# Performance work log

Hardware: AMD Instinct MI355X
Metric: run time of the kernel (lower is better)

## Reference

```python
import jax, jax.numpy as jnp
import numpy as np

N_NODES = 100000
N_ETYPES = 3
N_EDGES = 200000
IN, HID, OUT = 64, 128, 128


def setup_inputs() -> dict:
    key = jax.random.key(0)
    ks = jax.random.split(key, 7)
    x = jax.random.normal(ks[0], (N_NODES, IN), dtype=jnp.float32)
    edge_src = jax.random.randint(ks[1], (N_ETYPES, N_EDGES), 0, N_NODES, dtype=jnp.int32)
    edge_dst = jax.random.randint(ks[2], (N_ETYPES, N_EDGES), 0, N_NODES, dtype=jnp.int32)
    W1 = jax.random.normal(ks[3], (N_ETYPES, IN, HID), dtype=jnp.float32) * 0.05
    b1 = jax.random.normal(ks[4], (N_ETYPES, HID), dtype=jnp.float32) * 0.05
    W2 = jax.random.normal(ks[5], (N_ETYPES, HID, OUT), dtype=jnp.float32) * 0.05
    b2 = jax.random.normal(ks[6], (N_ETYPES, OUT), dtype=jnp.float32) * 0.05
    return {"x": x, "edge_src": edge_src, "edge_dst": edge_dst,
            "W1": W1, "b1": b1, "W2": W2, "b2": b2}


def _hetero_layer(h, edge_src, edge_dst, W, b):
    """Per-etype linear on src feats, mean-reduce per dst per etype, sum across etypes."""
    n = h.shape[0]
    # Wh: [n_etypes, N, H] -- dense per-etype transform (DGL applies Linear to all src nodes)
    Wh = jnp.einsum('nd,edh->enh', h, W) + b[:, None, :]

    def per_etype(Wh_e, src, dst):
        m = Wh_e[src]                                       # gather messages [E, H]
        s = jax.ops.segment_sum(m, dst, num_segments=n)     # scatter-sum   [N, H]
        cnt = jax.ops.segment_sum(jnp.ones((src.shape[0], 1), Wh_e.dtype), dst,
                                  num_segments=n)
        return s / jnp.maximum(cnt, 1.0)                    # mean reduce (0 if no in-edges)

    out = jax.vmap(per_etype)(Wh, edge_src, edge_dst)       # [n_etypes, N, H]
    return out.sum(axis=0)                                  # cross-type 'sum' aggregate


def reference(x, edge_src, edge_dst, W1, b1, W2, b2):
    h = _hetero_layer(x, edge_src, edge_dst, W1, b1)
    h = jax.nn.leaky_relu(h, negative_slope=0.01)
    return _hetero_layer(h, edge_src, edge_dst, W2, b2)
```

## Files before the change

### kernel.cpp

```cpp
#include <hip/hip_runtime.h>

#define NN 100000
#define NETY 3
#define EE 200000
#define DH 128
#define NBINS (NETY * NN)
#define CAP 32
#define SCAT_B ((NETY * EE + 255) / 256)

typedef __attribute__((ext_vector_type(8))) short short8;
typedef __attribute__((ext_vector_type(4))) short short4v;
typedef __attribute__((ext_vector_type(4))) float f32x4;

__device__ __forceinline__ float bf2f(unsigned short u) {
    return __uint_as_float(((unsigned int)u) << 16);
}
__device__ __forceinline__ unsigned short f2bf(float f) {
    unsigned int u = __float_as_uint(f);
    unsigned int r = ((u >> 16) & 1u) + 0x7fffu;
    return (unsigned short)((u + r) >> 16);
}

template <int K3>
__device__ __forceinline__ void wprep_body(const float* __restrict__ W,
                                           unsigned short* __restrict__ Wf, int tid) {
    int l = tid & 63;
    int nfks = tid >> 6;
    int nf = nfks & 7, ks = nfks >> 3;
    int k0 = ks * 32 + (l >> 4) * 8;
    int col = nf * 16 + (l & 15);
    short8 o;
    #pragma unroll
    for (int j = 0; j < 8; ++j)
        o[j] = (short)f2bf(W[(size_t)(k0 + j) * DH + col]);
    *reinterpret_cast<short8*>(Wf + (size_t)tid * 8) = o;
}

__global__ void scatter_wprep_kernel(const int* __restrict__ esrc,
                                     const int* __restrict__ edst,
                                     int* __restrict__ cnt, int* __restrict__ slots,
                                     const float* __restrict__ W1,
                                     const float* __restrict__ W2,
                                     unsigned short* __restrict__ Wf1,
                                     unsigned short* __restrict__ Wf2) {
    const int bid = blockIdx.x;
    if (bid < SCAT_B) {
        int tid = bid * 256 + threadIdx.x;
        if (tid < NETY * EE) {
            int e = tid / EE;
            int bin = e * NN + edst[tid];
            int pos = atomicAdd(&cnt[bin], 1);
            if (pos < CAP) slots[(size_t)bin * CAP + pos] = esrc[tid];
        }
    } else if (bid < SCAT_B + 12) {
        wprep_body<192>(W1, Wf1, (bid - SCAT_B) * 256 + threadIdx.x);
    } else {
        wprep_body<384>(W2, Wf2, (bid - SCAT_B - 12) * 256 + threadIdx.x);
    }
}

template <int DIN, bool BF16IN, bool BF16OUT>
__launch_bounds__(256)
__global__ void fused_layer_kernel(const void* __restrict__ feat_v,
                                   const int* __restrict__ slots,
                                   const int* __restrict__ cnt,
                                   const unsigned short* __restrict__ Wf,
                                   const float* __restrict__ bias,
                                   void* __restrict__ out_v) {
    constexpr int K3 = 3 * DIN;
    constexpr int NK = K3 / 32;
    constexpr int SP = K3 + 8;
    __shared__ unsigned short s_a[32 * SP];
    __shared__ float s_mask[NETY][32];

    const int t = threadIdx.x;
    const int n0 = blockIdx.x * 32;
    const int g = t >> 4, sub = t & 15;

    #pragma unroll
    for (int bi = 0; bi < 6; ++bi) {
        const int b = bi * 16 + g;
        const int nl = b & 31;
        const int e = b >> 5;
        const int bin = e * NN + n0 + nl;
        const int c = cnt[bin];
        const int sb = bin * CAP;
        const float inv = c > 0 ? 1.f / (float)c : 0.f;
        if constexpr (BF16IN) {
            const unsigned short* feat = (const unsigned short*)feat_v;
            float a[8] = {0.f, 0.f, 0.f, 0.f, 0.f, 0.f, 0.f, 0.f};
            for (int i = 0; i < c; ++i) {
                const int s = slots[sb + i];
                short8 u = *reinterpret_cast<const short8*>(feat + (size_t)s * DIN + sub * 8);
                #pragma unroll
                for (int j = 0; j < 8; ++j) {
                    float f = bf2f((unsigned short)u[j]);
                    a[j] += f > 0.f ? f : 0.01f * f;
                }
            }
            short8 o;
            #pragma unroll
            for (int j = 0; j < 8; ++j) o[j] = (short)f2bf(a[j] * inv);
            *reinterpret_cast<short8*>(&s_a[nl * SP + e * DIN + sub * 8]) = o;
        } else {
            const float* feat = (const float*)feat_v;
            float4 a = make_float4(0.f, 0.f, 0.f, 0.f);
            for (int i = 0; i < c; ++i) {
                const int s = slots[sb + i];
                float4 v = *reinterpret_cast<const float4*>(feat + (size_t)s * DIN + sub * 4);
                a.x += v.x; a.y += v.y; a.z += v.z; a.w += v.w;
            }
            short4v o;
            o[0] = (short)f2bf(a.x * inv);
            o[1] = (short)f2bf(a.y * inv);
            o[2] = (short)f2bf(a.z * inv);
            o[3] = (short)f2bf(a.w * inv);
            *reinterpret_cast<short4v*>(&s_a[nl * SP + e * DIN + sub * 4]) = o;
        }
        if (sub == 0) s_mask[e][nl] = c > 0 ? 1.f : 0.f;
    }
    __syncthreads();

    const int wv = t >> 6, l = t & 63;
    const int rowbase = (wv & 1) * 16;
    const int nfbase = (wv >> 1) * 4;
    const int lr = l & 15, lk = l >> 4;

    f32x4 acc[4] = {{0.f,0.f,0.f,0.f},{0.f,0.f,0.f,0.f},{0.f,0.f,0.f,0.f},{0.f,0.f,0.f,0.f}};
    const unsigned short* sa = &s_a[(rowbase + lr) * SP + lk * 8];

    #pragma unroll
    for (int ks = 0; ks < NK; ++ks) {
        short8 af = *reinterpret_cast<const short8*>(sa + ks * 32);
        const unsigned short* wb = Wf + ((size_t)(ks * 8 + nfbase) * 64 + l) * 8;
        #pragma unroll
        for (int nf = 0; nf < 4; ++nf) {
            short8 bf = *reinterpret_cast<const short8*>(wb + (size_t)nf * 64 * 8);
            acc[nf] = __builtin_amdgcn_mfma_f32_16x16x32_bf16(af, bf, acc[nf], 0, 0, 0);
        }
    }

    #pragma unroll
    for (int nf = 0; nf < 4; ++nf) {
        const int col = (nfbase + nf) * 16 + lr;
        const float b0 = bias[0 * DH + col];
        const float b1 = bias[1 * DH + col];
        const float b2 = bias[2 * DH + col];
        #pragma unroll
        for (int v = 0; v < 4; ++v) {
            const int row = rowbase + lk * 4 + v;
            const float val = acc[nf][v] + s_mask[0][row] * b0
                                         + s_mask[1][row] * b1
                                         + s_mask[2][row] * b2;
            if constexpr (BF16OUT)
                ((unsigned short*)out_v)[(size_t)(n0 + row) * DH + col] = f2bf(val);
            else
                ((float*)out_v)[(size_t)(n0 + row) * DH + col] = val;
        }
    }
}

extern "C" void kernel_launch(void* const* d_in, const int* in_sizes, int n_in,
                              void* d_out, int out_size, void* d_ws, size_t ws_size,
                              hipStream_t stream) {
    const float* x   = (const float*)d_in[0];
    const int* esrc  = (const int*)d_in[1];
    const int* edst  = (const int*)d_in[2];
    const float* W1  = (const float*)d_in[3];
    const float* b1  = (const float*)d_in[4];
    const float* W2  = (const float*)d_in[5];
    const float* b2  = (const float*)d_in[6];
    float* out = (float*)d_out;

    int* cnt    = (int*)d_ws;
    int* slots  = cnt + NBINS;
    unsigned short* Wf1 = (unsigned short*)(slots + (size_t)NBINS * CAP);
    unsigned short* Wf2 = Wf1 + 192 * DH;
    unsigned short* h   = Wf2 + 384 * DH;

    hipMemsetAsync(cnt, 0, sizeof(int) * NBINS, stream);

    scatter_wprep_kernel<<<SCAT_B + 12 + 24, 256, 0, stream>>>(
        esrc, edst, cnt, slots, W1, W2, Wf1, Wf2);

    fused_layer_kernel<64, false, true><<<NN / 32, 256, 0, stream>>>(
        x, slots, cnt, Wf1, b1, h);

    fused_layer_kernel<128, true, false><<<NN / 32, 256, 0, stream>>>(
        h, slots, cnt, Wf2, b2, out);
}
```

Before: 248.7 us.

## Convert x to bf16, process one node per thread-group with batched gathers

```diff
diff --git a/kernel.cpp b/kernel.cpp
--- a/kernel.cpp
+++ b/kernel.cpp
@@ -7,6 +7,8 @@
 #define NBINS (NETY * NN)
 #define CAP 32
 #define SCAT_B ((NETY * EE + 255) / 256)
+#define XPREP_T (NN * 64 / 8)
+#define XPREP_B ((XPREP_T + 255) / 256)
 
 typedef __attribute__((ext_vector_type(8))) short short8;
 typedef __attribute__((ext_vector_type(4))) short short4v;
@@ -19,6 +21,9 @@
     unsigned int u = __float_as_uint(f);
     unsigned int r = ((u >> 16) & 1u) + 0x7fffu;
     return (unsigned short)((u + r) >> 16);
+}
+__device__ __forceinline__ float lrelu(float f) {
+    return f > 0.f ? f : 0.01f * f;
 }
 
 template <int K3>
@@ -42,7 +47,9 @@
                                      const float* __restrict__ W1,
                                      const float* __restrict__ W2,
                                      unsigned short* __restrict__ Wf1,
-                                     unsigned short* __restrict__ Wf2) {
+                                     unsigned short* __restrict__ Wf2,
+                                     const float* __restrict__ x,
+                                     unsigned short* __restrict__ xb) {
     const int bid = blockIdx.x;
     if (bid < SCAT_B) {
         int tid = bid * 256 + threadIdx.x;
@@ -54,14 +61,34 @@
         }
     } else if (bid < SCAT_B + 12) {
         wprep_body<192>(W1, Wf1, (bid - SCAT_B) * 256 + threadIdx.x);
+    } else if (bid < SCAT_B + 36) {
+        wprep_body<384>(W2, Wf2, (bid - SCAT_B - 12) * 256 + threadIdx.x);
     } else {
-        wprep_body<384>(W2, Wf2, (bid - SCAT_B - 12) * 256 + threadIdx.x);
-    }
-}
-
-template <int DIN, bool BF16IN, bool BF16OUT>
+        int tid = (bid - SCAT_B - 36) * 256 + threadIdx.x;
+        if (tid < XPREP_T) {
+            const float* p = x + (size_t)tid * 8;
+            float4 v0 = *reinterpret_cast<const float4*>(p);
+            float4 v1 = *reinterpret_cast<const float4*>(p + 4);
+            short8 o;
+            o[0] = (short)f2bf(v0.x); o[1] = (short)f2bf(v0.y);
+            o[2] = (short)f2bf(v0.z); o[3] = (short)f2bf(v0.w);
+            o[4] = (short)f2bf(v1.x); o[5] = (short)f2bf(v1.y);
+            o[6] = (short)f2bf(v1.z); o[7] = (short)f2bf(v1.w);
+            *reinterpret_cast<short8*>(xb + (size_t)tid * 8) = o;
+        }
+    }
+}
+
+__device__ __forceinline__ int get_slot(int slo, const int* __restrict__ slots,
+                                        int sbase, int j) {
+    int v = __shfl(slo, j & 15, 16);
+    if (j >= 16) v = slots[sbase + j];
+    return v;
+}
+
+template <int DIN, bool LRELU_ON, bool BF16OUT>
 __launch_bounds__(256)
-__global__ void fused_layer_kernel(const void* __restrict__ feat_v,
+__global__ void fused_layer_kernel(const unsigned short* __restrict__ feat,
                                    const int* __restrict__ slots,
                                    const int* __restrict__ cnt,
                                    const unsigned short* __restrict__ Wf,
@@ -70,85 +97,156 @@
     constexpr int K3 = 3 * DIN;
     constexpr int NK = K3 / 32;
     constexpr int SP = K3 + 8;
-    __shared__ unsigned short s_a[32 * SP];
-    __shared__ float s_mask[NETY][32];
+    constexpr int CPL = DIN / 16;
+    __shared__ unsigned short s_a[16 * SP];
+    __shared__ float s_mask[NETY][16];
 
     const int t = threadIdx.x;
-    const int n0 = blockIdx.x * 32;
+    const int n0 = blockIdx.x * 16;
     const int g = t >> 4, sub = t & 15;
-
-    #pragma unroll
-    for (int bi = 0; bi < 6; ++bi) {
-        const int b = bi * 16 + g;
-        const int nl = b & 31;
-        const int e = b >> 5;
-        const int bin = e * NN + n0 + nl;
-        const int c = cnt[bin];
-        const int sb = bin * CAP;
-        const float inv = c > 0 ? 1.f / (float)c : 0.f;
-        if constexpr (BF16IN) {
-            const unsigned short* feat = (const unsigned short*)feat_v;
-            float a[8] = {0.f, 0.f, 0.f, 0.f, 0.f, 0.f, 0.f, 0.f};
-            for (int i = 0; i < c; ++i) {
-                const int s = slots[sb + i];
-                short8 u = *reinterpret_cast<const short8*>(feat + (size_t)s * DIN + sub * 8);
+    const int node = n0 + g;
+
+    int cb[NETY], sl[NETY];
+    #pragma unroll
+    for (int e = 0; e < NETY; ++e) cb[e] = cnt[e * NN + node];
+    #pragma unroll
+    for (int e = 0; e < NETY; ++e)
+        sl[e] = slots[(size_t)(e * NN + node) * CAP + sub];
+
+    int sidx[NETY][4];
+    float wgt[NETY][4];
+    #pragma unroll
+    for (int e = 0; e < NETY; ++e) {
+        const int c = cb[e];
+        const int cm1 = c > 0 ? c - 1 : 0;
+        #pragma unroll
+        for (int j = 0; j < 4; ++j) {
+            const int jj = j < c ? j : cm1;
+            int sv = __shfl(sl[e], jj, 16);
+            sidx[e][j] = c > 0 ? sv : 0;
+            wgt[e][j] = j < c ? 1.f : 0.f;
+        }
+    }
+
+    float a[NETY][CPL];
+    #pragma unroll
+    for (int e = 0; e < NETY; ++e)
+        #pragma unroll
+        for (int k = 0; k < CPL; ++k) a[e][k] = 0.f;
+
+    if constexpr (CPL == 8) {
+        short8 u[NETY][4];
+        #pragma unroll
+        for (int e = 0; e < NETY; ++e)
+            #pragma unroll
+            for (int j = 0; j < 4; ++j)
+                u[e][j] = *reinterpret_cast<const short8*>(
+                    feat + (size_t)sidx[e][j] * DIN + sub * 8);
+        #pragma unroll
+        for (int e = 0; e < NETY; ++e)
+            #pragma unroll
+            for (int j = 0; j < 4; ++j)
                 #pragma unroll
-                for (int j = 0; j < 8; ++j) {
-                    float f = bf2f((unsigned short)u[j]);
-                    a[j] += f > 0.f ? f : 0.01f * f;
+                for (int k = 0; k < 8; ++k) {
+                    float f = bf2f((unsigned short)u[e][j][k]);
+                    if constexpr (LRELU_ON) f = lrelu(f);
+                    a[e][k] = fmaf(wgt[e][j], f, a[e][k]);
+                }
+    } else {
+        short4v u[NETY][4];
+        #pragma unroll
+        for (int e = 0; e < NETY; ++e)
+            #pragma unroll
+            for (int j = 0; j < 4; ++j)
+                u[e][j] = *reinterpret_cast<const short4v*>(
+                    feat + (size_t)sidx[e][j] * DIN + sub * 4);
+        #pragma unroll
+        for (int e = 0; e < NETY; ++e)
+            #pragma unroll
+            for (int j = 0; j < 4; ++j)
+                #pragma unroll
+                for (int k = 0; k < 4; ++k) {
+                    float f = bf2f((unsigned short)u[e][j][k]);
+                    if constexpr (LRELU_ON) f = lrelu(f);
+                    a[e][k] = fmaf(wgt[e][j], f, a[e][k]);
+                }
+    }
+
+    #pragma unroll
+    for (int e = 0; e < NETY; ++e) {
+        const int c = cb[e];
+        if (c > 4) {
+            const int sbase = (e * NN + node) * CAP;
+            for (int j = 4; j < c; ++j) {
+                const int s = get_slot(sl[e], slots, sbase, j);
+                if constexpr (CPL == 8) {
+                    short8 u = *reinterpret_cast<const short8*>(
+                        feat + (size_t)s * DIN + sub * 8);
+                    #pragma unroll
+                    for (int k = 0; k < 8; ++k) {
+                        float f = bf2f((unsigned short)u[k]);
+                        if constexpr (LRELU_ON) f = lrelu(f);
+                        a[e][k] += f;
+                    }
+                } else {
+                    short4v u = *reinterpret_cast<const short4v*>(
+                        feat + (size_t)s * DIN + sub * 4);
+                    #pragma unroll
+                    for (int k = 0; k < 4; ++k) {
+                        float f = bf2f((unsigned short)u[k]);
+                        if constexpr (LRELU_ON) f = lrelu(f);
+                        a[e][k] += f;
+                    }
                 }
             }
+        }
+    }
+
+    #pragma unroll
+    for (int e = 0; e < NETY; ++e) {
+        const int c = cb[e];
+        const float inv = c > 0 ? 1.f / (float)c : 0.f;
+        if constexpr (CPL == 8) {
             short8 o;
             #pragma unroll
-            for (int j = 0; j < 8; ++j) o[j] = (short)f2bf(a[j] * inv);
-            *reinterpret_cast<short8*>(&s_a[nl * SP + e * DIN + sub * 8]) = o;
+            for (int k = 0; k < 8; ++k) o[k] = (short)f2bf(a[e][k] * inv);
+            *reinterpret_cast<short8*>(&s_a[g * SP + e * DIN + sub * 8]) = o;
         } else {
-            const float* feat = (const float*)feat_v;
-            float4 a = make_float4(0.f, 0.f, 0.f, 0.f);
-            for (int i = 0; i < c; ++i) {
-                const int s = slots[sb + i];
-                float4 v = *reinterpret_cast<const float4*>(feat + (size_t)s * DIN + sub * 4);
-                a.x += v.x; a.y += v.y; a.z += v.z; a.w += v.w;
-            }
             short4v o;
-            o[0] = (short)f2bf(a.x * inv);
-            o[1] = (short)f2bf(a.y * inv);
-            o[2] = (short)f2bf(a.z * inv);
-            o[3] = (short)f2bf(a.w * inv);
-            *reinterpret_cast<short4v*>(&s_a[nl * SP + e * DIN + sub * 4]) = o;
-        }
-        if (sub == 0) s_mask[e][nl] = c > 0 ? 1.f : 0.f;
+            #pragma unroll
+            for (int k = 0; k < 4; ++k) o[k] = (short)f2bf(a[e][k] * inv);
+            *reinterpret_cast<short4v*>(&s_a[g * SP + e * DIN + sub * 4]) = o;
+        }
+        if (sub == 0) s_mask[e][g] = c > 0 ? 1.f : 0.f;
     }
     __syncthreads();
 
     const int wv = t >> 6, l = t & 63;
-    const int rowbase = (wv & 1) * 16;
-    const int nfbase = (wv >> 1) * 4;
     const int lr = l & 15, lk = l >> 4;
 
-    f32x4 acc[4] = {{0.f,0.f,0.f,0.f},{0.f,0.f,0.f,0.f},{0.f,0.f,0.f,0.f},{0.f,0.f,0.f,0.f}};
-    const unsigned short* sa = &s_a[(rowbase + lr) * SP + lk * 8];
+    f32x4 acc[2] = {{0.f, 0.f, 0.f, 0.f}, {0.f, 0.f, 0.f, 0.f}};
+    const unsigned short* sa = &s_a[lr * SP + lk * 8];
 
     #pragma unroll
     for (int ks = 0; ks < NK; ++ks) {
         short8 af = *reinterpret_cast<const short8*>(sa + ks * 32);
-        const unsigned short* wb = Wf + ((size_t)(ks * 8 + nfbase) * 64 + l) * 8;
-        #pragma unroll
-        for (int nf = 0; nf < 4; ++nf) {
+        const unsigned short* wb = Wf + ((size_t)(ks * 8 + wv * 2) * 64 + l) * 8;
+        #pragma unroll
+        for (int nf = 0; nf < 2; ++nf) {
             short8 bf = *reinterpret_cast<const short8*>(wb + (size_t)nf * 64 * 8);
             acc[nf] = __builtin_amdgcn_mfma_f32_16x16x32_bf16(af, bf, acc[nf], 0, 0, 0);
         }
     }
 
     #pragma unroll
-    for (int nf = 0; nf < 4; ++nf) {
-        const int col = (nfbase + nf) * 16 + lr;
+    for (int nf = 0; nf < 2; ++nf) {
+        const int col = (wv * 2 + nf) * 16 + lr;
         const float b0 = bias[0 * DH + col];
         const float b1 = bias[1 * DH + col];
         const float b2 = bias[2 * DH + col];
         #pragma unroll
         for (int v = 0; v < 4; ++v) {
-            const int row = rowbase + lk * 4 + v;
+            const int row = lk * 4 + v;
             const float val = acc[nf][v] + s_mask[0][row] * b0
                                          + s_mask[1][row] * b1
                                          + s_mask[2][row] * b2;
@@ -177,15 +275,16 @@
     unsigned short* Wf1 = (unsigned short*)(slots + (size_t)NBINS * CAP);
     unsigned short* Wf2 = Wf1 + 192 * DH;
     unsigned short* h   = Wf2 + 384 * DH;
+    unsigned short* xb  = h + (size_t)NN * DH;
 
     hipMemsetAsync(cnt, 0, sizeof(int) * NBINS, stream);
 
-    scatter_wprep_kernel<<<SCAT_B + 12 + 24, 256, 0, stream>>>(
-        esrc, edst, cnt, slots, W1, W2, Wf1, Wf2);
-
-    fused_layer_kernel<64, false, true><<<NN / 32, 256, 0, stream>>>(
-        x, slots, cnt, Wf1, b1, h);
-
-    fused_layer_kernel<128, true, false><<<NN / 32, 256, 0, stream>>>(
+    scatter_wprep_kernel<<<SCAT_B + 36 + XPREP_B, 256, 0, stream>>>(
+        esrc, edst, cnt, slots, W1, W2, Wf1, Wf2, x, xb);
+
+    fused_layer_kernel<64, false, true><<<NN / 16, 256, 0, stream>>>(
+        xb, slots, cnt, Wf1, b1, h);
+
+    fused_layer_kernel<128, true, false><<<NN / 16, 256, 0, stream>>>(
         h, slots, cnt, Wf2, b2, out);
 }
```

After: 200.5 us. 1.24x faster.
